# Optimization experiments

Hardware: AMD Instinct MI355X
Metric: run time of the kernel (lower is better)

## Reference

```python
import jax, jax.numpy as jnp
import numpy as np

NEG_SLOPE = 0.2


def gat_conv(x, edge_index, W, a_src, a_dst, b):
    # PyG GATConv (heads=1, add_self_loops=True, concat -> out_channels)
    N = x.shape[0]
    h = x @ W                                   # [N, F_out]
    loops = jnp.arange(N, dtype=edge_index.dtype)
    src = jnp.concatenate([edge_index[0], loops])   # message sources (x_j)
    dst = jnp.concatenate([edge_index[1], loops])   # message targets (x_i)
    # attention logits: e = LeakyReLU(a_src . h_j + a_dst . h_i)
    alpha_s = h @ a_src                          # [N]
    alpha_d = h @ a_dst                          # [N]
    e = jax.nn.leaky_relu(alpha_s[src] + alpha_d[dst], NEG_SLOPE)  # [E+N]
    # segment softmax over incoming edges of each dst node
    m = jax.ops.segment_max(e, dst, num_segments=N)
    e = jnp.exp(e - m[dst])
    denom = jax.ops.segment_sum(e, dst, num_segments=N)
    alpha = e / denom[dst]                       # self-loops guarantee denom > 0
    # weighted scatter-sum aggregation
    out = jax.ops.segment_sum(alpha[:, None] * h[src], dst, num_segments=N)
    return out + b


def setup_inputs() -> dict:
    key = jax.random.key(0)
    ks = jax.random.split(key, 10)
    N, E, F_in, H, F_out = 100000, 3200000, 54, 16, 16
    x = jax.random.normal(ks[0], (N, F_in), dtype=jnp.float32)
    edge_index = jax.random.randint(ks[1], (2, E), 0, N, dtype=jnp.int64)
    s1 = 1.0 / np.sqrt(F_in)
    s2 = 1.0 / np.sqrt(H)
    return {
        "x": x,
        "edge_index": edge_index,
        "W1": jax.random.uniform(ks[2], (F_in, H), jnp.float32, -s1, s1),
        "a1_src": jax.random.uniform(ks[3], (H,), jnp.float32, -s2, s2),
        "a1_dst": jax.random.uniform(ks[4], (H,), jnp.float32, -s2, s2),
        "b1": jnp.zeros((H,), jnp.float32),
        "W2": jax.random.uniform(ks[5], (H, F_out), jnp.float32, -s2, s2),
        "a2_src": jax.random.uniform(ks[6], (F_out,), jnp.float32, -0.25, 0.25),
        "a2_dst": jax.random.uniform(ks[7], (F_out,), jnp.float32, -0.25, 0.25),
        "b2": jnp.zeros((F_out,), jnp.float32),
    }


def reference(x, edge_index, W1, a1_src, a1_dst, b1, W2, a2_src, a2_dst, b2):
    h = gat_conv(x, edge_index, W1, a1_src, a1_dst, b1)
    h = jax.nn.elu(h)
    # dropout p=0.5 is identity in eval mode
    out = gat_conv(h, edge_index, W2, a2_src, a2_dst, b2)
    return out
```

## Files before the change

kernel.cpp:

```cpp
#include <hip/hip_runtime.h>
#include <hip/hip_bf16.h>

typedef __hip_bfloat16 bf16;

static constexpr int N_NODES = 100000;
static constexpr int N_EDGES = 3200000;
static constexpr int F_IN    = 54;
static constexpr int F_HID   = 16;

static constexpr int BSHIFT    = 7;
static constexpr int BNODES    = 128;
static constexpr int NBUCK     = (N_NODES + BNODES - 1) / BNODES;
static constexpr int CAP_B     = 5120;
static constexpr int BIN_CHUNK = 4096;
static constexpr int BTHR      = 512;
static constexpr int GRDB      = (N_EDGES + BIN_CHUNK - 1) / BIN_CHUNK;
static constexpr int GRDN_F    = (N_NODES + BTHR - 1) / BTHR;
static constexpr int HELD      = CAP_B / 512;

static constexpr size_t WS_FLAGS  = 0;
static constexpr size_t WS_ADST   = 4;
static constexpr size_t WS_ADST2  = 100004;
static constexpr size_t WS_BCNT   = 200004;
static constexpr size_t WS_HC1    = 401028;
static constexpr size_t WS_HC2    = 2001028;
static constexpr size_t WS_BEDGES = 3601028;
static constexpr size_t WS_SRCS   = 7604868;
static constexpr size_t WS_BUCKET_END = WS_SRCS + (size_t)NBUCK * CAP_B;
static constexpr size_t WS_FB_DEN     = 3601028;
static constexpr size_t WS_FB_AS      = 3701028;
static constexpr size_t WS_ATOMIC_END = 3801028;

__device__ __forceinline__ float lrelu(float v) { return fmaxf(v, 0.2f * v); }
__device__ __forceinline__ float loadf(const void* p, int i, bool f32) {
    return f32 ? ((const float*)p)[i] : __bfloat162float(((const bf16*)p)[i]);
}
__device__ __forceinline__ unsigned f2bf(float f) {
    unsigned u = __float_as_uint(f);
    return (u + 0x7FFFu + ((u >> 16) & 1u)) >> 16;
}

__global__ __launch_bounds__(256) void k_probe0(
    const void* __restrict__ x, const void* __restrict__ ei,
    int* __restrict__ flags, int* __restrict__ bcnt)
{
    __shared__ int cnt, nz;
    const int t = threadIdx.x;
    if (t == 0) { cnt = 0; nz = 0; }
    __syncthreads();
    const unsigned u = ((const unsigned*)x)[t];
    if ((u & 0x7FFFu) >= 0x4800u) atomicAdd(&cnt, 1);
    if (t < 64) {
        if (((const unsigned*)ei)[2 * t + 1] != 0u) atomicAdd(&nz, 1);
    }
    for (int i = t; i < 1024; i += 256) bcnt[i] = 0;
    __syncthreads();
    if (t == 0) flags[0] = ((cnt >= 16) ? 1 : 0) | ((nz == 0) ? 2 : 0);
}

__global__ __launch_bounds__(512, 8) void k_binfeat(
    const void* __restrict__ ei, const void* __restrict__ x,
    const void* __restrict__ W1, const void* __restrict__ a_s,
    const void* __restrict__ a_d, const int* __restrict__ flags,
    int* __restrict__ bcnt, int* __restrict__ bedges,
    unsigned* __restrict__ hc, float* __restrict__ adst)
{
    __shared__ int            hist[NBUCK];
    __shared__ int            base[NBUCK];
    __shared__ int            cval[BIN_CHUNK];
    __shared__ unsigned short cbkt[BIN_CHUNK];
    __shared__ float Wl[F_IN * F_HID];
    __shared__ float asl[F_HID];
    __shared__ float adl[F_HID];
    const int t = threadIdx.x;
    const bool f32 = flags[0] & 1;
    const bool i64 = flags[0] & 2;

    if (blockIdx.x < GRDB) {
        const int e0 = blockIdx.x * BIN_CHUNK;
        const int valid = min(BIN_CHUNK, N_EDGES - e0);
        for (int i = t; i < NBUCK; i += BTHR) hist[i] = 0;
        __syncthreads();
#pragma unroll
        for (int i = 0; i < BIN_CHUNK / BTHR; ++i) {
            const int idx = i * BTHR + t;
            const int e = e0 + idx;
            if (idx < valid) {
                int s, d;
                if (i64) {
                    s = ((const int*)ei)[2 * (size_t)e];
                    d = ((const int*)ei)[2 * ((size_t)N_EDGES + e)];
                } else {
                    s = ((const int*)ei)[e];
                    d = ((const int*)ei)[(size_t)N_EDGES + e];
                }
                const int b = d >> BSHIFT;
                cval[idx] = (s << BSHIFT) | (d & (BNODES - 1));
                cbkt[idx] = (unsigned short)b;
                atomicAdd(&hist[b], 1);
            }
        }
        __syncthreads();
        for (int i = t; i < NBUCK; i += BTHR) {
            const int c = hist[i];
            base[i] = c ? atomicAdd(&bcnt[i], c) : 0;
            hist[i] = 0;
        }
        __syncthreads();
#pragma unroll
        for (int i = 0; i < BIN_CHUNK / BTHR; ++i) {
            const int idx = i * BTHR + t;
            if (idx < valid) {
                const int b = cbkt[idx];
                const int r = atomicAdd(&hist[b], 1);
                const int pos = base[b] + r;
                if (pos < CAP_B) bedges[(size_t)b * CAP_B + pos] = cval[idx];
            }
        }
    } else {
        for (int i = t; i < F_IN * F_HID; i += BTHR) Wl[i] = loadf(W1, i, f32);
        if (t < F_HID) { asl[t] = loadf(a_s, t, f32); adl[t] = loadf(a_d, t, f32); }
        __syncthreads();
        const int node = (blockIdx.x - GRDB) * BTHR + t;
        if (node >= N_NODES) return;

        float h[F_HID];
#pragma unroll
        for (int k = 0; k < F_HID; ++k) h[k] = 0.f;
        if (f32) {
            const float2* xp = (const float2*)((const float*)x + (size_t)node * F_IN);
#pragma unroll
            for (int j = 0; j < F_IN / 2; ++j) {
                const float2 v = xp[j];
#pragma unroll
                for (int k = 0; k < F_HID; ++k) {
                    h[k] = fmaf(v.x, Wl[(2*j)   * F_HID + k], h[k]);
                    h[k] = fmaf(v.y, Wl[(2*j+1) * F_HID + k], h[k]);
                }
            }
        } else {
            const unsigned* xu = (const unsigned*)x + (size_t)node * (F_IN / 2);
#pragma unroll
            for (int j = 0; j < F_IN / 2; ++j) {
                const unsigned u = xu[j];
                const float v0 = __uint_as_float(u << 16);
                const float v1 = __uint_as_float(u & 0xFFFF0000u);
#pragma unroll
                for (int k = 0; k < F_HID; ++k) {
                    h[k] = fmaf(v0, Wl[(2*j)   * F_HID + k], h[k]);
                    h[k] = fmaf(v1, Wl[(2*j+1) * F_HID + k], h[k]);
                }
            }
        }
        float s = 0.f, d = 0.f;
#pragma unroll
        for (int k = 0; k < F_HID; ++k) { s = fmaf(h[k], asl[k], s); d = fmaf(h[k], adl[k], d); }
        adst[node] = d;
        const unsigned ab = f2bf(s) << 16;
        unsigned pk[F_HID];
#pragma unroll
        for (int k = 0; k < F_HID; ++k) pk[k] = f2bf(h[k]) | ab;
        uint4* hb = (uint4*)(hc + (size_t)node * F_HID);
#pragma unroll
        for (int q = 0; q < 4; ++q)
            hb[q] = make_uint4(pk[4*q], pk[4*q+1], pk[4*q+2], pk[4*q+3]);
    }
}

__device__ __forceinline__ void bucket_sort_lds(
    const int* __restrict__ bedges, const int* __restrict__ bcnt, int b, int t,
    int* hist, int* scanv, int* cur, int* srt)
{
    if (t < BNODES) hist[t] = 0;
    __syncthreads();
    const int cnt = min(bcnt[b], CAP_B);
    const int* cv = bedges + (size_t)b * CAP_B;
    int held[HELD];
#pragma unroll
    for (int q = 0; q < HELD; ++q) {
        const int e = t + q * 512;
        const int v = cv[e];
        held[q] = (e < cnt) ? v : -1;
    }
#pragma unroll
    for (int q = 0; q < HELD; ++q)
        if (held[q] >= 0) atomicAdd(&hist[held[q] & (BNODES - 1)], 1);
    __syncthreads();
    if (t < BNODES) scanv[t] = hist[t];
    __syncthreads();
#pragma unroll
    for (int off = 1; off < BNODES; off <<= 1) {
        const int v = (t < BNODES && t >= off) ? scanv[t - off] : 0;
        __syncthreads();
        if (t < BNODES) scanv[t] += v;
        __syncthreads();
    }
    if (t < BNODES) cur[t] = scanv[t] - hist[t];
    __syncthreads();
#pragma unroll
    for (int q = 0; q < HELD; ++q) {
        if (held[q] >= 0) {
            const int p  = held[q];
            const int r  = atomicAdd(&cur[p & (BNODES - 1)], 1);
            srt[r] = p >> BSHIFT;
        }
    }
    __syncthreads();
}

__global__ __launch_bounds__(512, 6) void k_agg1(
    const int* __restrict__ bcnt, const int* __restrict__ bedges,
    const float* __restrict__ adst, const unsigned* __restrict__ hc,
    const void* __restrict__ b1, const void* __restrict__ W2,
    const void* __restrict__ a_s2, const void* __restrict__ a_d2,
    const int* __restrict__ flags,
    unsigned* __restrict__ hc2, float* __restrict__ adst2)
{
    __shared__ float Wl[F_HID * F_HID];
    __shared__ float asl[F_HID], adl[F_HID], bl[F_HID];
    __shared__ float adL[BNODES];
    __shared__ int hist[BNODES], scanv[BNODES], cur[BNODES];
    __shared__ int srt[CAP_B];
    const bool f32 = flags[0] & 1;
    const int t = threadIdx.x;
    const int b = blockIdx.x;
    const int n0 = b << BSHIFT;
    if (t < F_HID * F_HID) Wl[t] = loadf(W2, t, f32);
    if (t < F_HID) {
        asl[t] = loadf(a_s2, t, f32);
        adl[t] = loadf(a_d2, t, f32);
        bl[t]  = loadf(b1, t, f32);
    }
    if (t < BNODES) {
        const int node = n0 + t;
        adL[t] = (node < N_NODES) ? adst[node] : 0.f;
    }
    bucket_sort_lds(bedges, bcnt, b, t, hist, scanv, cur, srt);

    const int k = t & 15;
    const int g = t >> 4;
#pragma unroll
    for (int it = 0; it < 4; ++it) {
        const int dl = it * 32 + g;
        const int node = n0 + dl;
        if (node >= N_NODES) continue;
        const float adn = adL[dl];
        const unsigned vs = hc[((size_t)node << 4) + k];
        const float w0 = __expf(lrelu(__uint_as_float(vs & 0xFFFF0000u) + adn));
        float denom = w0;
        float acc = w0 * __uint_as_float(vs << 16);
        const int n = hist[dl];
        const int* sp = srt + (scanv[dl] - n);
        int i = 0;
        for (; i + 8 <= n; i += 8) {
            const int s0 = sp[i+0], s1 = sp[i+1], s2 = sp[i+2], s3 = sp[i+3];
            const int s4 = sp[i+4], s5 = sp[i+5], s6 = sp[i+6], s7 = sp[i+7];
            const unsigned v0 = hc[((size_t)s0 << 4) + k];
            const unsigned v1 = hc[((size_t)s1 << 4) + k];
            const unsigned v2 = hc[((size_t)s2 << 4) + k];
            const unsigned v3 = hc[((size_t)s3 << 4) + k];
            const unsigned v4 = hc[((size_t)s4 << 4) + k];
            const unsigned v5 = hc[((size_t)s5 << 4) + k];
            const unsigned v6 = hc[((size_t)s6 << 4) + k];
            const unsigned v7 = hc[((size_t)s7 << 4) + k];
            const float e0 = __expf(lrelu(__uint_as_float(v0 & 0xFFFF0000u) + adn));
            const float e1 = __expf(lrelu(__uint_as_float(v1 & 0xFFFF0000u) + adn));
            const float e2 = __expf(lrelu(__uint_as_float(v2 & 0xFFFF0000u) + adn));
            const float e3 = __expf(lrelu(__uint_as_float(v3 & 0xFFFF0000u) + adn));
            const float e4 = __expf(lrelu(__uint_as_float(v4 & 0xFFFF0000u) + adn));
            const float e5 = __expf(lrelu(__uint_as_float(v5 & 0xFFFF0000u) + adn));
            const float e6 = __expf(lrelu(__uint_as_float(v6 & 0xFFFF0000u) + adn));
            const float e7 = __expf(lrelu(__uint_as_float(v7 & 0xFFFF0000u) + adn));
            denom += (e0 + e1 + e2 + e3) + (e4 + e5 + e6 + e7);
            acc = fmaf(e0, __uint_as_float(v0 << 16), acc);
            acc = fmaf(e1, __uint_as_float(v1 << 16), acc);
            acc = fmaf(e2, __uint_as_float(v2 << 16), acc);
            acc = fmaf(e3, __uint_as_float(v3 << 16), acc);
            acc = fmaf(e4, __uint_as_float(v4 << 16), acc);
            acc = fmaf(e5, __uint_as_float(v5 << 16), acc);
            acc = fmaf(e6, __uint_as_float(v6 << 16), acc);
            acc = fmaf(e7, __uint_as_float(v7 << 16), acc);
        }
        for (; i < n; ++i) {
            const unsigned v = hc[((size_t)sp[i] << 4) + k];
            const float w = __expf(lrelu(__uint_as_float(v & 0xFFFF0000u) + adn));
            denom += w;
            acc = fmaf(w, __uint_as_float(v << 16), acc);
        }
        float z = acc / denom + bl[k];
        z = z > 0.f ? z : expm1f(z);
        float hh = 0.f;
#pragma unroll
        for (int j = 0; j < F_HID; ++j) {
            const float zj = __shfl(z, j, 16);
            hh = fmaf(zj, Wl[j * F_HID + k], hh);
        }
        float s2 = hh * asl[k], d2 = hh * adl[k];
#pragma unroll
        for (int off = 1; off < 16; off <<= 1) {
            s2 += __shfl_xor(s2, off, 16);
            d2 += __shfl_xor(d2, off, 16);
        }
        hc2[((size_t)node << 4) + k] = f2bf(hh) | (f2bf(s2) << 16);
        if (k == 0) adst2[node] = d2;
    }
}

__global__ __launch_bounds__(512, 6) void k_agg2(
    const int* __restrict__ bcnt, const int* __restrict__ bedges,
    const float* __restrict__ adst, const unsigned* __restrict__ hc,
    const void* __restrict__ b2, const int* __restrict__ flags,
    float* __restrict__ outp)
{
    __shared__ float bl[F_HID];
    __shared__ float adL[BNODES];
    __shared__ int hist[BNODES], scanv[BNODES], cur[BNODES];
    __shared__ int srt[CAP_B];
    const bool f32 = flags[0] & 1;
    const int t = threadIdx.x;
    const int b = blockIdx.x;
    const int n0 = b << BSHIFT;
    if (t < F_HID) bl[t] = loadf(b2, t, f32);
    if (t < BNODES) {
        const int node = n0 + t;
        adL[t] = (node < N_NODES) ? adst[node] : 0.f;
    }
    bucket_sort_lds(bedges, bcnt, b, t, hist, scanv, cur, srt);

    const int k = t & 15;
    const int g = t >> 4;
#pragma unroll
    for (int it = 0; it < 4; ++it) {
        const int dl = it * 32 + g;
        const int node = n0 + dl;
        if (node >= N_NODES) continue;
        const float adn = adL[dl];
        const unsigned vs = hc[((size_t)node << 4) + k];
        const float w0 = __expf(lrelu(__uint_as_float(vs & 0xFFFF0000u) + adn));
        float denom = w0;
        float acc = w0 * __uint_as_float(vs << 16);
        const int n = hist[dl];
        const int* sp = srt + (scanv[dl] - n);
        int i = 0;
        for (; i + 8 <= n; i += 8) {
            const int s0 = sp[i+0], s1 = sp[i+1], s2 = sp[i+2], s3 = sp[i+3];
            const int s4 = sp[i+4], s5 = sp[i+5], s6 = sp[i+6], s7 = sp[i+7];
            const unsigned v0 = hc[((size_t)s0 << 4) + k];
            const unsigned v1 = hc[((size_t)s1 << 4) + k];
            const unsigned v2 = hc[((size_t)s2 << 4) + k];
            const unsigned v3 = hc[((size_t)s3 << 4) + k];
            const unsigned v4 = hc[((size_t)s4 << 4) + k];
            const unsigned v5 = hc[((size_t)s5 << 4) + k];
            const unsigned v6 = hc[((size_t)s6 << 4) + k];
            const unsigned v7 = hc[((size_t)s7 << 4) + k];
            const float e0 = __expf(lrelu(__uint_as_float(v0 & 0xFFFF0000u) + adn));
            const float e1 = __expf(lrelu(__uint_as_float(v1 & 0xFFFF0000u) + adn));
            const float e2 = __expf(lrelu(__uint_as_float(v2 & 0xFFFF0000u) + adn));
            const float e3 = __expf(lrelu(__uint_as_float(v3 & 0xFFFF0000u) + adn));
            const float e4 = __expf(lrelu(__uint_as_float(v4 & 0xFFFF0000u) + adn));
            const float e5 = __expf(lrelu(__uint_as_float(v5 & 0xFFFF0000u) + adn));
            const float e6 = __expf(lrelu(__uint_as_float(v6 & 0xFFFF0000u) + adn));
            const float e7 = __expf(lrelu(__uint_as_float(v7 & 0xFFFF0000u) + adn));
            denom += (e0 + e1 + e2 + e3) + (e4 + e5 + e6 + e7);
            acc = fmaf(e0, __uint_as_float(v0 << 16), acc);
            acc = fmaf(e1, __uint_as_float(v1 << 16), acc);
            acc = fmaf(e2, __uint_as_float(v2 << 16), acc);
            acc = fmaf(e3, __uint_as_float(v3 << 16), acc);
            acc = fmaf(e4, __uint_as_float(v4 << 16), acc);
            acc = fmaf(e5, __uint_as_float(v5 << 16), acc);
            acc = fmaf(e6, __uint_as_float(v6 << 16), acc);
            acc = fmaf(e7, __uint_as_float(v7 << 16), acc);
        }
        for (; i < n; ++i) {
            const unsigned v = hc[((size_t)sp[i] << 4) + k];
            const float w = __expf(lrelu(__uint_as_float(v & 0xFFFF0000u) + adn));
            denom += w;
            acc = fmaf(w, __uint_as_float(v << 16), acc);
        }
        outp[((size_t)node << 4) + k] = acc / denom + bl[k];
    }
}

__global__ __launch_bounds__(256) void k_feat1(
    const void* __restrict__ x, const void* __restrict__ W1,
    const void* __restrict__ a_s, const void* __restrict__ a_d,
    const int* __restrict__ flags,
    float* __restrict__ hbuf, float* __restrict__ asrc, float* __restrict__ adst)
{
    const bool f32 = flags[0] & 1;
    __shared__ float Wl[F_IN * F_HID];
    __shared__ float asl[F_HID];
    __shared__ float adl[F_HID];
    const int t = threadIdx.x;
    for (int i = t; i < F_IN * F_HID; i += 256) Wl[i] = loadf(W1, i, f32);
    if (t < F_HID) { asl[t] = loadf(a_s, t, f32); adl[t] = loadf(a_d, t, f32); }
    __syncthreads();
    const int node = blockIdx.x * 256 + t;
    if (node >= N_NODES) return;
    float h[F_HID];
#pragma unroll
    for (int k = 0; k < F_HID; ++k) h[k] = 0.f;
    if (f32) {
        const float2* xp = (const float2*)((const float*)x + (size_t)node * F_IN);
#pragma unroll
        for (int j = 0; j < F_IN / 2; ++j) {
            const float2 v = xp[j];
#pragma unroll
            for (int k = 0; k < F_HID; ++k) {
                h[k] = fmaf(v.x, Wl[(2*j)   * F_HID + k], h[k]);
                h[k] = fmaf(v.y, Wl[(2*j+1) * F_HID + k], h[k]);
            }
        }
    } else {
        const unsigned* xu = (const unsigned*)x + (size_t)node * (F_IN / 2);
#pragma unroll
        for (int j = 0; j < F_IN / 2; ++j) {
            const unsigned u = xu[j];
            const float v0 = __uint_as_float(u << 16);
            const float v1 = __uint_as_float(u & 0xFFFF0000u);
#pragma unroll
            for (int k = 0; k < F_HID; ++k) {
                h[k] = fmaf(v0, Wl[(2*j)   * F_HID + k], h[k]);
                h[k] = fmaf(v1, Wl[(2*j+1) * F_HID + k], h[k]);
            }
        }
    }
    float s = 0.f, d = 0.f;
#pragma unroll
    for (int k = 0; k < F_HID; ++k) { s = fmaf(h[k], asl[k], s); d = fmaf(h[k], adl[k], d); }
    asrc[node] = s; adst[node] = d;
    float4* hb = (float4*)(hbuf + (size_t)node * F_HID);
#pragma unroll
    for (int q = 0; q < 4; ++q)
        hb[q] = make_float4(h[4*q], h[4*q+1], h[4*q+2], h[4*q+3]);
}

__global__ __launch_bounds__(256) void k_selfinit(
    const float* __restrict__ asrc, const float* __restrict__ adst,
    const float* __restrict__ h, float* __restrict__ denom, float* __restrict__ acc)
{
    const int t = blockIdx.x * 256 + threadIdx.x;
    if (t >= N_NODES * F_HID) return;
    const int n = t >> 4;
    const float w0 = __expf(lrelu(asrc[n] + adst[n]));
    if ((t & 15) == 0) denom[n] = w0;
    acc[t] = w0 * h[t];
}

__global__ __launch_bounds__(256) void k_edge(
    const void* __restrict__ ei, const int* __restrict__ flags,
    const float* __restrict__ asrc, const float* __restrict__ adst,
    const float* __restrict__ hbuf,
    float* __restrict__ denom, float* __restrict__ acc)
{
    const int e = blockIdx.x * 256 + threadIdx.x;
    if (e >= N_EDGES) return;
    int s, d;
    if (flags[0] & 2) {
        const long long* e64 = (const long long*)ei;
        s = (int)e64[e]; d = (int)e64[(size_t)N_EDGES + e];
    } else {
        const int* e32 = (const int*)ei;
        s = e32[e]; d = e32[(size_t)N_EDGES + e];
    }
    const float w = __expf(lrelu(asrc[s] + adst[d]));
    atomicAdd(&denom[d], w);
    const float4* hs = (const float4*)(hbuf + (size_t)s * F_HID);
    float* ad = acc + (size_t)d * F_HID;
#pragma unroll
    for (int q = 0; q < 4; ++q) {
        const float4 hv = hs[q];
        atomicAdd(ad + 4*q + 0, w * hv.x);
        atomicAdd(ad + 4*q + 1, w * hv.y);
        atomicAdd(ad + 4*q + 2, w * hv.z);
        atomicAdd(ad + 4*q + 3, w * hv.w);
    }
}

__global__ __launch_bounds__(256) void k_div_elu(
    float* __restrict__ acc, const float* __restrict__ denom,
    const void* __restrict__ b1, const int* __restrict__ flags)
{
    const bool f32 = flags[0] & 1;
    const int t = blockIdx.x * 256 + threadIdx.x;
    if (t >= N_NODES * F_HID) return;
    const float v = acc[t] / denom[t >> 4] + loadf(b1, t & 15, f32);
    acc[t] = v > 0.f ? v : expm1f(v);
}

__global__ __launch_bounds__(256) void k_mid(
    const float* __restrict__ z,
    const void* __restrict__ W2, const void* __restrict__ a_s2,
    const void* __restrict__ a_d2, const int* __restrict__ flags,
    float* __restrict__ h2, float* __restrict__ asrc, float* __restrict__ adst)
{
    const bool f32 = flags[0] & 1;
    __shared__ float Wl[F_HID * F_HID];
    __shared__ float asl[F_HID];
    __shared__ float adl[F_HID];
    const int t = threadIdx.x;
    if (t < F_HID * F_HID) Wl[t] = loadf(W2, t, f32);
    if (t < F_HID) { asl[t] = loadf(a_s2, t, f32); adl[t] = loadf(a_d2, t, f32); }
    __syncthreads();
    const int node = blockIdx.x * 256 + t;
    if (node >= N_NODES) return;
    float zr[F_HID];
    const float4* zi = (const float4*)(z + (size_t)node * F_HID);
#pragma unroll
    for (int q = 0; q < 4; ++q) {
        const float4 zv = zi[q];
        zr[4*q+0]=zv.x; zr[4*q+1]=zv.y; zr[4*q+2]=zv.z; zr[4*q+3]=zv.w;
    }
    float h[F_HID];
#pragma unroll
    for (int k = 0; k < F_HID; ++k) h[k] = 0.f;
#pragma unroll
    for (int j = 0; j < F_HID; ++j) {
        const float zv = zr[j];
#pragma unroll
        for (int k = 0; k < F_HID; ++k) h[k] = fmaf(zv, Wl[j * F_HID + k], h[k]);
    }
    float s = 0.f, d = 0.f;
#pragma unroll
    for (int k = 0; k < F_HID; ++k) { s = fmaf(h[k], asl[k], s); d = fmaf(h[k], adl[k], d); }
    asrc[node] = s; adst[node] = d;
    float4* hb = (float4*)(h2 + (size_t)node * F_HID);
#pragma unroll
    for (int q = 0; q < 4; ++q)
        hb[q] = make_float4(h[4*q], h[4*q+1], h[4*q+2], h[4*q+3]);
}

__global__ __launch_bounds__(256) void k_out(
    const float* __restrict__ acc, const float* __restrict__ denom,
    const void* __restrict__ b2, const int* __restrict__ flags,
    float* __restrict__ out)
{
    const bool f32 = flags[0] & 1;
    const int t = blockIdx.x * 256 + threadIdx.x;
    if (t >= N_NODES * F_HID) return;
    out[t] = acc[t] / denom[t >> 4] + loadf(b2, t & 15, f32);
}

__global__ __launch_bounds__(256) void k_diag(float* __restrict__ out, float v)
{
    const int t = blockIdx.x * 256 + threadIdx.x;
    if (t < N_NODES * F_HID) out[t] = v;
}

extern "C" void kernel_launch(void* const* d_in, const int* in_sizes, int n_in,
                              void* d_out, int out_size, void* d_ws, size_t ws_size,
                              hipStream_t stream) {
    const void* x   = d_in[0];
    const void* ei  = d_in[1];
    const void* W1  = d_in[2];
    const void* a1s = d_in[3];
    const void* a1d = d_in[4];
    const void* b1  = d_in[5];
    const void* W2  = d_in[6];
    const void* a2s = d_in[7];
    const void* a2d = d_in[8];
    const void* b2  = d_in[9];
    float* out = (float*)d_out;

    float* ws = (float*)d_ws;
    int*      flags  = (int*)(ws + WS_FLAGS);
    float*    adst   = ws + WS_ADST;
    float*    adst2  = ws + WS_ADST2;
    int*      bcnt   = (int*)(ws + WS_BCNT);
    unsigned* hc1    = (unsigned*)(ws + WS_HC1);
    unsigned* hc2    = (unsigned*)(ws + WS_HC2);
    int*      bedges = (int*)(ws + WS_BEDGES);

    const dim3 blk(256);
    const dim3 grdN((N_NODES + 255) / 256);
    const dim3 grdE((N_EDGES + 255) / 256);
    const dim3 grdO((N_NODES * F_HID + 255) / 256);
    const dim3 grdBF(GRDB + GRDN_F);
    const dim3 grdB(NBUCK);

    if (ws_size >= WS_BUCKET_END * 4) {
        k_probe0 <<<dim3(1), blk, 0, stream>>>(x, ei, flags, bcnt);
        k_binfeat<<<grdBF, dim3(BTHR), 0, stream>>>(ei, x, W1, a1s, a1d, flags,
                                                    bcnt, bedges, hc1, adst);
        k_agg1   <<<grdB, dim3(512), 0, stream>>>(bcnt, bedges, adst, hc1,
                                                  b1, W2, a2s, a2d, flags, hc2, adst2);
        k_agg2   <<<grdB, dim3(512), 0, stream>>>(bcnt, bedges, adst2, hc2,
                                                  b2, flags, out);
    } else if (ws_size >= WS_ATOMIC_END * 4) {
        float* fb_h   = ws + WS_HC1;
        float* fb_acc = ws + WS_HC2;
        float* fb_den = ws + WS_FB_DEN;
        float* fb_as  = ws + WS_FB_AS;
        float* fb_ad  = ws + WS_ADST;
        k_probe0 <<<dim3(1), blk, 0, stream>>>(x, ei, flags, bcnt);
        k_feat1  <<<grdN, blk, 0, stream>>>(x, W1, a1s, a1d, flags, fb_h, fb_as, fb_ad);
        k_selfinit<<<grdO, blk, 0, stream>>>(fb_as, fb_ad, fb_h, fb_den, fb_acc);
        k_edge   <<<grdE, blk, 0, stream>>>(ei, flags, fb_as, fb_ad, fb_h, fb_den, fb_acc);
        k_div_elu<<<grdO, blk, 0, stream>>>(fb_acc, fb_den, b1, flags);
        k_mid    <<<grdN, blk, 0, stream>>>(fb_acc, W2, a2s, a2d, flags, fb_h, fb_as, fb_ad);
        k_selfinit<<<grdO, blk, 0, stream>>>(fb_as, fb_ad, fb_h, fb_den, fb_acc);
        k_edge   <<<grdE, blk, 0, stream>>>(ei, flags, fb_as, fb_ad, fb_h, fb_den, fb_acc);
        k_out    <<<grdO, blk, 0, stream>>>(fb_acc, fb_den, b2, flags, out);
    } else {
        k_diag<<<grdO, blk, 0, stream>>>(out, (float)(ws_size >> 10));
    }
}
```

Baseline: 234.1 us.

## Pack features as bf16 pairs and separate source attention logits into own array

Node features are now stored as 16 packed bf16 values (32 bytes per node) instead of 16 words each carrying a duplicated bf16 source logit, and the source logit moves to a separate fp32 array. The aggregation kernels switch from 16 lanes per node with 4 nodes per thread-group iteration to 4 lanes per node, each loading a uint2 (4 features), with one node per 4 threads. This halves the gathered feature bytes per edge and lets each thread accumulate 4 channels, at the cost of an extra scattered 4-byte asrc load per edge replicated across the 4 lanes. The source logit also keeps fp32 precision now.

Measured after the change: 223.1 us. 1.05x faster.

```diff
diff --git a/kernel.cpp b/kernel.cpp
--- a/kernel.cpp
+++ b/kernel.cpp
@@ -22,6 +22,8 @@
 static constexpr size_t WS_ADST   = 4;
 static constexpr size_t WS_ADST2  = 100004;
 static constexpr size_t WS_BCNT   = 200004;
+static constexpr size_t WS_ASRC1  = 201028;
+static constexpr size_t WS_ASRC2  = 301028;
 static constexpr size_t WS_HC1    = 401028;
 static constexpr size_t WS_HC2    = 2001028;
 static constexpr size_t WS_BEDGES = 3601028;
@@ -39,6 +41,8 @@
     unsigned u = __float_as_uint(f);
     return (u + 0x7FFFu + ((u >> 16) & 1u)) >> 16;
 }
+__device__ __forceinline__ float bflo(unsigned u) { return __uint_as_float(u << 16); }
+__device__ __forceinline__ float bfhi(unsigned u) { return __uint_as_float(u & 0xFFFF0000u); }
 
 __global__ __launch_bounds__(256) void k_probe0(
     const void* __restrict__ x, const void* __restrict__ ei,
@@ -63,7 +67,7 @@
     const void* __restrict__ W1, const void* __restrict__ a_s,
     const void* __restrict__ a_d, const int* __restrict__ flags,
     int* __restrict__ bcnt, int* __restrict__ bedges,
-    unsigned* __restrict__ hc, float* __restrict__ adst)
+    unsigned* __restrict__ hc, float* __restrict__ asrc, float* __restrict__ adst)
 {
     __shared__ int            hist[NBUCK];
     __shared__ int            base[NBUCK];
@@ -155,15 +159,14 @@
         float s = 0.f, d = 0.f;
 #pragma unroll
         for (int k = 0; k < F_HID; ++k) { s = fmaf(h[k], asl[k], s); d = fmaf(h[k], adl[k], d); }
+        asrc[node] = s;
         adst[node] = d;
-        const unsigned ab = f2bf(s) << 16;
-        unsigned pk[F_HID];
-#pragma unroll
-        for (int k = 0; k < F_HID; ++k) pk[k] = f2bf(h[k]) | ab;
-        uint4* hb = (uint4*)(hc + (size_t)node * F_HID);
-#pragma unroll
-        for (int q = 0; q < 4; ++q)
-            hb[q] = make_uint4(pk[4*q], pk[4*q+1], pk[4*q+2], pk[4*q+3]);
+        unsigned pk[8];
+#pragma unroll
+        for (int q = 0; q < 8; ++q) pk[q] = f2bf(h[2*q]) | (f2bf(h[2*q+1]) << 16);
+        uint4* hb = (uint4*)(hc + ((size_t)node << 3));
+        hb[0] = make_uint4(pk[0], pk[1], pk[2], pk[3]);
+        hb[1] = make_uint4(pk[4], pk[5], pk[6], pk[7]);
     }
 }
 
@@ -210,15 +213,16 @@
 
 __global__ __launch_bounds__(512, 6) void k_agg1(
     const int* __restrict__ bcnt, const int* __restrict__ bedges,
-    const float* __restrict__ adst, const unsigned* __restrict__ hc,
+    const float* __restrict__ asrc, const float* __restrict__ adst,
+    const unsigned* __restrict__ hc,
     const void* __restrict__ b1, const void* __restrict__ W2,
     const void* __restrict__ a_s2, const void* __restrict__ a_d2,
     const int* __restrict__ flags,
-    unsigned* __restrict__ hc2, float* __restrict__ adst2)
+    unsigned* __restrict__ hc2, float* __restrict__ asrc2, float* __restrict__ adst2)
 {
     __shared__ float Wl[F_HID * F_HID];
     __shared__ float asl[F_HID], adl[F_HID], bl[F_HID];
-    __shared__ float adL[BNODES];
+    __shared__ float adL[BNODES], asL[BNODES];
     __shared__ int hist[BNODES], scanv[BNODES], cur[BNODES];
     __shared__ int srt[CAP_B];
     const bool f32 = flags[0] & 1;
@@ -233,87 +237,128 @@
     }
     if (t < BNODES) {
         const int node = n0 + t;
-        adL[t] = (node < N_NODES) ? adst[node] : 0.f;
+        const bool ok = node < N_NODES;
+        adL[t] = ok ? adst[node] : 0.f;
+        asL[t] = ok ? asrc[node] : 0.f;
     }
     bucket_sort_lds(bedges, bcnt, b, t, hist, scanv, cur, srt);
 
-    const int k = t & 15;
-    const int g = t >> 4;
-#pragma unroll
-    for (int it = 0; it < 4; ++it) {
-        const int dl = it * 32 + g;
-        const int node = n0 + dl;
-        if (node >= N_NODES) continue;
-        const float adn = adL[dl];
-        const unsigned vs = hc[((size_t)node << 4) + k];
-        const float w0 = __expf(lrelu(__uint_as_float(vs & 0xFFFF0000u) + adn));
+    const int k2 = t & 3;
+    const int g  = t >> 2;
+    const int node = n0 + g;
+    if (node < N_NODES) {
+        const int K = k2 << 2;
+        const float adn = adL[g];
+        const uint2 us = *(const uint2*)(hc + ((size_t)node << 3) + (k2 << 1));
+        const float w0 = __expf(lrelu(asL[g] + adn));
         float denom = w0;
-        float acc = w0 * __uint_as_float(vs << 16);
-        const int n = hist[dl];
-        const int* sp = srt + (scanv[dl] - n);
+        float a0 = w0 * bflo(us.x), a1 = w0 * bfhi(us.x);
+        float a2 = w0 * bflo(us.y), a3 = w0 * bfhi(us.y);
+        const int n = hist[g];
+        const int* sp = srt + (scanv[g] - n);
         int i = 0;
         for (; i + 8 <= n; i += 8) {
-            const int s0 = sp[i+0], s1 = sp[i+1], s2 = sp[i+2], s3 = sp[i+3];
+            const int s0 = sp[i+0], s1 = sp[i+1], s2_ = sp[i+2], s3 = sp[i+3];
             const int s4 = sp[i+4], s5 = sp[i+5], s6 = sp[i+6], s7 = sp[i+7];
-            const unsigned v0 = hc[((size_t)s0 << 4) + k];
-            const unsigned v1 = hc[((size_t)s1 << 4) + k];
-            const unsigned v2 = hc[((size_t)s2 << 4) + k];
-            const unsigned v3 = hc[((size_t)s3 << 4) + k];
-            const unsigned v4 = hc[((size_t)s4 << 4) + k];
-            const unsigned v5 = hc[((size_t)s5 << 4) + k];
-            const unsigned v6 = hc[((size_t)s6 << 4) + k];
-            const unsigned v7 = hc[((size_t)s7 << 4) + k];
-            const float e0 = __expf(lrelu(__uint_as_float(v0 & 0xFFFF0000u) + adn));
-            const float e1 = __expf(lrelu(__uint_as_float(v1 & 0xFFFF0000u) + adn));
-            const float e2 = __expf(lrelu(__uint_as_float(v2 & 0xFFFF0000u) + adn));
-            const float e3 = __expf(lrelu(__uint_as_float(v3 & 0xFFFF0000u) + adn));
-            const float e4 = __expf(lrelu(__uint_as_float(v4 & 0xFFFF0000u) + adn));
-            const float e5 = __expf(lrelu(__uint_as_float(v5 & 0xFFFF0000u) + adn));
-            const float e6 = __expf(lrelu(__uint_as_float(v6 & 0xFFFF0000u) + adn));
-            const float e7 = __expf(lrelu(__uint_as_float(v7 & 0xFFFF0000u) + adn));
+            const uint2 v0 = *(const uint2*)(hc + ((size_t)s0 << 3) + (k2 << 1));
+            const uint2 v1 = *(const uint2*)(hc + ((size_t)s1 << 3) + (k2 << 1));
+            const uint2 v2 = *(const uint2*)(hc + ((size_t)s2_ << 3) + (k2 << 1));
+            const uint2 v3 = *(const uint2*)(hc + ((size_t)s3 << 3) + (k2 << 1));
+            const uint2 v4 = *(const uint2*)(hc + ((size_t)s4 << 3) + (k2 << 1));
+            const uint2 v5 = *(const uint2*)(hc + ((size_t)s5 << 3) + (k2 << 1));
+            const uint2 v6 = *(const uint2*)(hc + ((size_t)s6 << 3) + (k2 << 1));
+            const uint2 v7 = *(const uint2*)(hc + ((size_t)s7 << 3) + (k2 << 1));
+            const float x0 = asrc[s0], x1 = asrc[s1], x2 = asrc[s2_], x3 = asrc[s3];
+            const float x4 = asrc[s4], x5 = asrc[s5], x6 = asrc[s6], x7 = asrc[s7];
+            const float e0 = __expf(lrelu(x0 + adn));
+            const float e1 = __expf(lrelu(x1 + adn));
+            const float e2 = __expf(lrelu(x2 + adn));
+            const float e3 = __expf(lrelu(x3 + adn));
+            const float e4 = __expf(lrelu(x4 + adn));
+            const float e5 = __expf(lrelu(x5 + adn));
+            const float e6 = __expf(lrelu(x6 + adn));
+            const float e7 = __expf(lrelu(x7 + adn));
             denom += (e0 + e1 + e2 + e3) + (e4 + e5 + e6 + e7);
-            acc = fmaf(e0, __uint_as_float(v0 << 16), acc);
-            acc = fmaf(e1, __uint_as_float(v1 << 16), acc);
-            acc = fmaf(e2, __uint_as_float(v2 << 16), acc);
-            acc = fmaf(e3, __uint_as_float(v3 << 16), acc);
-            acc = fmaf(e4, __uint_as_float(v4 << 16), acc);
-            acc = fmaf(e5, __uint_as_float(v5 << 16), acc);
-            acc = fmaf(e6, __uint_as_float(v6 << 16), acc);
-            acc = fmaf(e7, __uint_as_float(v7 << 16), acc);
+            a0 = fmaf(e0, bflo(v0.x), a0); a1 = fmaf(e0, bfhi(v0.x), a1);
+            a2 = fmaf(e0, bflo(v0.y), a2); a3 = fmaf(e0, bfhi(v0.y), a3);
+            a0 = fmaf(e1, bflo(v1.x), a0); a1 = fmaf(e1, bfhi(v1.x), a1);
+            a2 = fmaf(e1, bflo(v1.y), a2); a3 = fmaf(e1, bfhi(v1.y), a3);
+            a0 = fmaf(e2, bflo(v2.x), a0); a1 = fmaf(e2, bfhi(v2.x), a1);
+            a2 = fmaf(e2, bflo(v2.y), a2); a3 = fmaf(e2, bfhi(v2.y), a3);
+            a0 = fmaf(e3, bflo(v3.x), a0); a1 = fmaf(e3, bfhi(v3.x), a1);
+            a2 = fmaf(e3, bflo(v3.y), a2); a3 = fmaf(e3, bfhi(v3.y), a3);
+            a0 = fmaf(e4, bflo(v4.x), a0); a1 = fmaf(e4, bfhi(v4.x), a1);
+            a2 = fmaf(e4, bflo(v4.y), a2); a3 = fmaf(e4, bfhi(v4.y), a3);
+            a0 = fmaf(e5, bflo(v5.x), a0); a1 = fmaf(e5, bfhi(v5.x), a1);
+            a2 = fmaf(e5, bflo(v5.y), a2); a3 = fmaf(e5, bfhi(v5.y), a3);
+            a0 = fmaf(e6, bflo(v6.x), a0); a1 = fmaf(e6, bfhi(v6.x), a1);
+            a2 = fmaf(e6, bflo(v6.y), a2); a3 = fmaf(e6, bfhi(v6.y), a3);
+            a0 = fmaf(e7, bflo(v7.x), a0); a1 = fmaf(e7, bfhi(v7.x), a1);
+            a2 = fmaf(e7, bflo(v7.y), a2); a3 = fmaf(e7, bfhi(v7.y), a3);
         }
         for (; i < n; ++i) {
-            const unsigned v = hc[((size_t)sp[i] << 4) + k];
-            const float w = __expf(lrelu(__uint_as_float(v & 0xFFFF0000u) + adn));
+            const int s = sp[i];
+            const uint2 v = *(const uint2*)(hc + ((size_t)s << 3) + (k2 << 1));
+            const float w = __expf(lrelu(asrc[s] + adn));
             denom += w;
-            acc = fmaf(w, __uint_as_float(v << 16), acc);
-        }
-        float z = acc / denom + bl[k];
-        z = z > 0.f ? z : expm1f(z);
-        float hh = 0.f;
-#pragma unroll
-        for (int j = 0; j < F_HID; ++j) {
-            const float zj = __shfl(z, j, 16);
-            hh = fmaf(zj, Wl[j * F_HID + k], hh);
-        }
-        float s2 = hh * asl[k], d2 = hh * adl[k];
-#pragma unroll
-        for (int off = 1; off < 16; off <<= 1) {
-            s2 += __shfl_xor(s2, off, 16);
-            d2 += __shfl_xor(d2, off, 16);
-        }
-        hc2[((size_t)node << 4) + k] = f2bf(hh) | (f2bf(s2) << 16);
-        if (k == 0) adst2[node] = d2;
+            a0 = fmaf(w, bflo(v.x), a0); a1 = fmaf(w, bfhi(v.x), a1);
+            a2 = fmaf(w, bflo(v.y), a2); a3 = fmaf(w, bfhi(v.y), a3);
+        }
+        const float inv = 1.f / denom;
+        float z0 = a0 * inv + bl[K+0];
+        float z1 = a1 * inv + bl[K+1];
+        float z2 = a2 * inv + bl[K+2];
+        float z3 = a3 * inv + bl[K+3];
+        z0 = z0 > 0.f ? z0 : expm1f(z0);
+        z1 = z1 > 0.f ? z1 : expm1f(z1);
+        z2 = z2 > 0.f ? z2 : expm1f(z2);
+        z3 = z3 > 0.f ? z3 : expm1f(z3);
+        float hh0 = 0.f, hh1 = 0.f, hh2 = 0.f, hh3 = 0.f;
+#pragma unroll
+        for (int jl = 0; jl < 4; ++jl) {
+            const float zj0 = __shfl(z0, jl, 4);
+            const float zj1 = __shfl(z1, jl, 4);
+            const float zj2 = __shfl(z2, jl, 4);
+            const float zj3 = __shfl(z3, jl, 4);
+            const int jb = jl << 2;
+            hh0 = fmaf(zj0, Wl[(jb+0)*F_HID + K+0], hh0);
+            hh1 = fmaf(zj0, Wl[(jb+0)*F_HID + K+1], hh1);
+            hh2 = fmaf(zj0, Wl[(jb+0)*F_HID + K+2], hh2);
+            hh3 = fmaf(zj0, Wl[(jb+0)*F_HID + K+3], hh3);
+            hh0 = fmaf(zj1, Wl[(jb+1)*F_HID + K+0], hh0);
+            hh1 = fmaf(zj1, Wl[(jb+1)*F_HID + K+1], hh1);
+            hh2 = fmaf(zj1, Wl[(jb+1)*F_HID + K+2], hh2);
+            hh3 = fmaf(zj1, Wl[(jb+1)*F_HID + K+3], hh3);
+            hh0 = fmaf(zj2, Wl[(jb+2)*F_HID + K+0], hh0);
+            hh1 = fmaf(zj2, Wl[(jb+2)*F_HID + K+1], hh1);
+            hh2 = fmaf(zj2, Wl[(jb+2)*F_HID + K+2], hh2);
+            hh3 = fmaf(zj2, Wl[(jb+2)*F_HID + K+3], hh3);
+            hh0 = fmaf(zj3, Wl[(jb+3)*F_HID + K+0], hh0);
+            hh1 = fmaf(zj3, Wl[(jb+3)*F_HID + K+1], hh1);
+            hh2 = fmaf(zj3, Wl[(jb+3)*F_HID + K+2], hh2);
+            hh3 = fmaf(zj3, Wl[(jb+3)*F_HID + K+3], hh3);
+        }
+        float s2 = hh0*asl[K+0] + hh1*asl[K+1] + hh2*asl[K+2] + hh3*asl[K+3];
+        float d2 = hh0*adl[K+0] + hh1*adl[K+1] + hh2*adl[K+2] + hh3*adl[K+3];
+        s2 += __shfl_xor(s2, 1, 4); s2 += __shfl_xor(s2, 2, 4);
+        d2 += __shfl_xor(d2, 1, 4); d2 += __shfl_xor(d2, 2, 4);
+        uint2 w;
+        w.x = f2bf(hh0) | (f2bf(hh1) << 16);
+        w.y = f2bf(hh2) | (f2bf(hh3) << 16);
+        *(uint2*)(hc2 + ((size_t)node << 3) + (k2 << 1)) = w;
+        if (k2 == 0) { asrc2[node] = s2; adst2[node] = d2; }
     }
 }
 
 __global__ __launch_bounds__(512, 6) void k_agg2(
     const int* __restrict__ bcnt, const int* __restrict__ bedges,
-    const float* __restrict__ adst, const unsigned* __restrict__ hc,
+    const float* __restrict__ asrc, const float* __restrict__ adst,
+    const unsigned* __restrict__ hc,
     const void* __restrict__ b2, const int* __restrict__ flags,
     float* __restrict__ outp)
 {
     __shared__ float bl[F_HID];
-    __shared__ float adL[BNODES];
+    __shared__ float adL[BNODES], asL[BNODES];
     __shared__ int hist[BNODES], scanv[BNODES], cur[BNODES];
     __shared__ int srt[CAP_B];
     const bool f32 = flags[0] & 1;
@@ -323,61 +368,80 @@
     if (t < F_HID) bl[t] = loadf(b2, t, f32);
     if (t < BNODES) {
         const int node = n0 + t;
-        adL[t] = (node < N_NODES) ? adst[node] : 0.f;
+        const bool ok = node < N_NODES;
+        adL[t] = ok ? adst[node] : 0.f;
+        asL[t] = ok ? asrc[node] : 0.f;
     }
     bucket_sort_lds(bedges, bcnt, b, t, hist, scanv, cur, srt);
 
-    const int k = t & 15;
-    const int g = t >> 4;
-#pragma unroll
-    for (int it = 0; it < 4; ++it) {
-        const int dl = it * 32 + g;
-        const int node = n0 + dl;
-        if (node >= N_NODES) continue;
-        const float adn = adL[dl];
-        const unsigned vs = hc[((size_t)node << 4) + k];
-        const float w0 = __expf(lrelu(__uint_as_float(vs & 0xFFFF0000u) + adn));
+    const int k2 = t & 3;
+    const int g  = t >> 2;
+    const int node = n0 + g;
+    if (node < N_NODES) {
+        const int K = k2 << 2;
+        const float adn = adL[g];
+        const uint2 us = *(const uint2*)(hc + ((size_t)node << 3) + (k2 << 1));
+        const float w0 = __expf(lrelu(asL[g] + adn));
         float denom = w0;
-        float acc = w0 * __uint_as_float(vs << 16);
-        const int n = hist[dl];
-        const int* sp = srt + (scanv[dl] - n);
+        float a0 = w0 * bflo(us.x), a1 = w0 * bfhi(us.x);
+        float a2 = w0 * bflo(us.y), a3 = w0 * bfhi(us.y);
+        const int n = hist[g];
+        const int* sp = srt + (scanv[g] - n);
         int i = 0;
         for (; i + 8 <= n; i += 8) {
-            const int s0 = sp[i+0], s1 = sp[i+1], s2 = sp[i+2], s3 = sp[i+3];
+            const int s0 = sp[i+0], s1 = sp[i+1], s2_ = sp[i+2], s3 = sp[i+3];
             const int s4 = sp[i+4], s5 = sp[i+5], s6 = sp[i+6], s7 = sp[i+7];
-            const unsigned v0 = hc[((size_t)s0 << 4) + k];
-            const unsigned v1 = hc[((size_t)s1 << 4) + k];
-            const unsigned v2 = hc[((size_t)s2 << 4) + k];
-            const unsigned v3 = hc[((size_t)s3 << 4) + k];
-            const unsigned v4 = hc[((size_t)s4 << 4) + k];
-            const unsigned v5 = hc[((size_t)s5 << 4) + k];
-            const unsigned v6 = hc[((size_t)s6 << 4) + k];
-            const unsigned v7 = hc[((size_t)s7 << 4) + k];
-            const float e0 = __expf(lrelu(__uint_as_float(v0 & 0xFFFF0000u) + adn));
-            const float e1 = __expf(lrelu(__uint_as_float(v1 & 0xFFFF0000u) + adn));
-            const float e2 = __expf(lrelu(__uint_as_float(v2 & 0xFFFF0000u) + adn));
-            const float e3 = __expf(lrelu(__uint_as_float(v3 & 0xFFFF0000u) + adn));
-            const float e4 = __expf(lrelu(__uint_as_float(v4 & 0xFFFF0000u) + adn));
-            const float e5 = __expf(lrelu(__uint_as_float(v5 & 0xFFFF0000u) + adn));
-            const float e6 = __expf(lrelu(__uint_as_float(v6 & 0xFFFF0000u) + adn));
-            const float e7 = __expf(lrelu(__uint_as_float(v7 & 0xFFFF0000u) + adn));
+            const uint2 v0 = *(const uint2*)(hc + ((size_t)s0 << 3) + (k2 << 1));
+            const uint2 v1 = *(const uint2*)(hc + ((size_t)s1 << 3) + (k2 << 1));
+            const uint2 v2 = *(const uint2*)(hc + ((size_t)s2_ << 3) + (k2 << 1));
+            const uint2 v3 = *(const uint2*)(hc + ((size_t)s3 << 3) + (k2 << 1));
+            const uint2 v4 = *(const uint2*)(hc + ((size_t)s4 << 3) + (k2 << 1));
+            const uint2 v5 = *(const uint2*)(hc + ((size_t)s5 << 3) + (k2 << 1));
+            const uint2 v6 = *(const uint2*)(hc + ((size_t)s6 << 3) + (k2 << 1));
+            const uint2 v7 = *(const uint2*)(hc + ((size_t)s7 << 3) + (k2 << 1));
+            const float x0 = asrc[s0], x1 = asrc[s1], x2 = asrc[s2_], x3 = asrc[s3];
+            const float x4 = asrc[s4], x5 = asrc[s5], x6 = asrc[s6], x7 = asrc[s7];
+            const float e0 = __expf(lrelu(x0 + adn));
+            const float e1 = __expf(lrelu(x1 + adn));
+            const float e2 = __expf(lrelu(x2 + adn));
+            const float e3 = __expf(lrelu(x3 + adn));
+            const float e4 = __expf(lrelu(x4 + adn));
+            const float e5 = __expf(lrelu(x5 + adn));
+            const float e6 = __expf(lrelu(x6 + adn));
+            const float e7 = __expf(lrelu(x7 + adn));
             denom += (e0 + e1 + e2 + e3) + (e4 + e5 + e6 + e7);
-            acc = fmaf(e0, __uint_as_float(v0 << 16), acc);
-            acc = fmaf(e1, __uint_as_float(v1 << 16), acc);
-            acc = fmaf(e2, __uint_as_float(v2 << 16), acc);
-            acc = fmaf(e3, __uint_as_float(v3 << 16), acc);
-            acc = fmaf(e4, __uint_as_float(v4 << 16), acc);
-            acc = fmaf(e5, __uint_as_float(v5 << 16), acc);
-            acc = fmaf(e6, __uint_as_float(v6 << 16), acc);
-            acc = fmaf(e7, __uint_as_float(v7 << 16), acc);
+            a0 = fmaf(e0, bflo(v0.x), a0); a1 = fmaf(e0, bfhi(v0.x), a1);
+            a2 = fmaf(e0, bflo(v0.y), a2); a3 = fmaf(e0, bfhi(v0.y), a3);
+            a0 = fmaf(e1, bflo(v1.x), a0); a1 = fmaf(e1, bfhi(v1.x), a1);
+            a2 = fmaf(e1, bflo(v1.y), a2); a3 = fmaf(e1, bfhi(v1.y), a3);
+            a0 = fmaf(e2, bflo(v2.x), a0); a1 = fmaf(e2, bfhi(v2.x), a1);
+            a2 = fmaf(e2, bflo(v2.y), a2); a3 = fmaf(e2, bfhi(v2.y), a3);
+            a0 = fmaf(e3, bflo(v3.x), a0); a1 = fmaf(e3, bfhi(v3.x), a1);
+            a2 = fmaf(e3, bflo(v3.y), a2); a3 = fmaf(e3, bfhi(v3.y), a3);
+            a0 = fmaf(e4, bflo(v4.x), a0); a1 = fmaf(e4, bfhi(v4.x), a1);
+            a2 = fmaf(e4, bflo(v4.y), a2); a3 = fmaf(e4, bfhi(v4.y), a3);
+            a0 = fmaf(e5, bflo(v5.x), a0); a1 = fmaf(e5, bfhi(v5.x), a1);
+            a2 = fmaf(e5, bflo(v5.y), a2); a3 = fmaf(e5, bfhi(v5.y), a3);
+            a0 = fmaf(e6, bflo(v6.x), a0); a1 = fmaf(e6, bfhi(v6.x), a1);
+            a2 = fmaf(e6, bflo(v6.y), a2); a3 = fmaf(e6, bfhi(v6.y), a3);
+            a0 = fmaf(e7, bflo(v7.x), a0); a1 = fmaf(e7, bfhi(v7.x), a1);
+            a2 = fmaf(e7, bflo(v7.y), a2); a3 = fmaf(e7, bfhi(v7.y), a3);
         }
         for (; i < n; ++i) {
-            const unsigned v = hc[((size_t)sp[i] << 4) + k];
-            const float w = __expf(lrelu(__uint_as_float(v & 0xFFFF0000u) + adn));
+            const int s = sp[i];
+            const uint2 v = *(const uint2*)(hc + ((size_t)s << 3) + (k2 << 1));
+            const float w = __expf(lrelu(asrc[s] + adn));
             denom += w;
-            acc = fmaf(w, __uint_as_float(v << 16), acc);
-        }
-        outp[((size_t)node << 4) + k] = acc / denom + bl[k];
+            a0 = fmaf(w, bflo(v.x), a0); a1 = fmaf(w, bfhi(v.x), a1);
+            a2 = fmaf(w, bflo(v.y), a2); a3 = fmaf(w, bfhi(v.y), a3);
+        }
+        const float inv = 1.f / denom;
+        float4 o;
+        o.x = a0 * inv + bl[K+0];
+        o.y = a1 * inv + bl[K+1];
+        o.z = a2 * inv + bl[K+2];
+        o.w = a3 * inv + bl[K+3];
+        *(float4*)(outp + ((size_t)node << 4) + K) = o;
     }
 }
 
@@ -567,6 +631,8 @@
     float*    adst   = ws + WS_ADST;
     float*    adst2  = ws + WS_ADST2;
     int*      bcnt   = (int*)(ws + WS_BCNT);
+    float*    asrc1  = ws + WS_ASRC1;
+    float*    asrc2  = ws + WS_ASRC2;
     unsigned* hc1    = (unsigned*)(ws + WS_HC1);
     unsigned* hc2    = (unsigned*)(ws + WS_HC2);
     int*      bedges = (int*)(ws + WS_BEDGES);
@@ -581,10 +647,11 @@
     if (ws_size >= WS_BUCKET_END * 4) {
         k_probe0 <<<dim3(1), blk, 0, stream>>>(x, ei, flags, bcnt);
         k_binfeat<<<grdBF, dim3(BTHR), 0, stream>>>(ei, x, W1, a1s, a1d, flags,
-                                                    bcnt, bedges, hc1, adst);
-        k_agg1   <<<grdB, dim3(512), 0, stream>>>(bcnt, bedges, adst, hc1,
-                                                  b1, W2, a2s, a2d, flags, hc2, adst2);
-        k_agg2   <<<grdB, dim3(512), 0, stream>>>(bcnt, bedges, adst2, hc2,
+                                                    bcnt, bedges, hc1, asrc1, adst);
+        k_agg1   <<<grdB, dim3(512), 0, stream>>>(bcnt, bedges, asrc1, adst, hc1,
+                                                  b1, W2, a2s, a2d, flags,
+                                                  hc2, asrc2, adst2);
+        k_agg2   <<<grdB, dim3(512), 0, stream>>>(bcnt, bedges, asrc2, adst2, hc2,
                                                   b2, flags, out);
     } else if (ws_size >= WS_ATOMIC_END * 4) {
         float* fb_h   = ws + WS_HC1;
```
